# Kernel optimization log

Hardware: AMD Instinct MI355X
Metric: run time of the kernel (lower is better)

The kernel has to match this reference:

```python
import jax, jax.numpy as jnp
import numpy as np

TEMPERATURE = 0.1


def setup_inputs() -> dict:
    key = jax.random.key(0)
    k1, k2 = jax.random.split(key)
    B, D = 4096, 128
    z_i = jax.random.normal(k1, (B, D), dtype=jnp.float32)
    z_j = jax.random.normal(k2, (B, D), dtype=jnp.float32)
    return {"z_i": z_i, "z_j": z_j}


def reference(z_i, z_j):
    B = z_i.shape[0]
    n = 2 * B
    z = jnp.concatenate([z_i, z_j], axis=0)            # [2B, D]
    sim = jnp.matmul(z, z.T) / TEMPERATURE             # [2B, 2B]
    # positives: diag(sim, +B) and diag(sim, -B)
    pos = jnp.concatenate([jnp.diagonal(sim, B), jnp.diagonal(sim, -B)])[:, None]  # [2B, 1]
    # negatives: sim with diagonal removed, row-wise -> [2B, 2B-1]
    # strided trick equivalent to sim[~eye].reshape(n, n-1)
    neg = sim.ravel()[:-1].reshape(n - 1, n + 1)[:, 1:].reshape(n, n - 1)
    logits = jnp.concatenate([pos, neg], axis=1)       # [2B, 2B]
    # cross-entropy with labels all zero (positive in column 0)
    loss = jnp.mean(jax.nn.logsumexp(logits, axis=1) - logits[:, 0])
    return loss
```

## Files before the change

### kernel.cpp

```cpp
#include <hip/hip_runtime.h>
#include <hip/hip_bf16.h>
#include <stdint.h>

#define N_TOT  8192
#define BHALF  4096
#define DDIM   128
#define NSPLIT 16

typedef short bf16x8 __attribute__((ext_vector_type(8)));
typedef float f32x4  __attribute__((ext_vector_type(4)));

__device__ __forceinline__ float ex2(float x) { return __builtin_amdgcn_exp2f(x); }

#define SCALE_C 3.798282440185f

__device__ __forceinline__ ushort2 cvt2(float a, float b) {
    __hip_bfloat162 h = __float22bfloat162_rn(make_float2(a, b));
    return *reinterpret_cast<ushort2*>(&h);
}

__device__ __forceinline__ bf16x8 cvt8(float4 lo, float4 hi) {
    union { bf16x8 v; ushort2 u[4]; } r;
    r.u[0] = cvt2(lo.x * SCALE_C, lo.y * SCALE_C);
    r.u[1] = cvt2(lo.z * SCALE_C, lo.w * SCALE_C);
    r.u[2] = cvt2(hi.x * SCALE_C, hi.y * SCALE_C);
    r.u[3] = cvt2(hi.z * SCALE_C, hi.w * SCALE_C);
    return r.v;
}

struct StageRegs { float4 v[4]; };

__device__ __forceinline__ StageRegs stage_load(const float* __restrict__ zi,
                                                const float* __restrict__ zj,
                                                int colBase, int ch, int tid) {
    StageRegs s;
    #pragma unroll
    for (int it = 0; it < 2; ++it) {
        int idx  = it * 512 + tid;
        int col  = idx >> 4, g = idx & 15;
        int gcol = colBase + ch * 64 + col;
        const float* cp = (gcol < BHALF) ? zi + gcol * DDIM
                                         : zj + (gcol - BHALF) * DDIM;
        s.v[it * 2]     = *reinterpret_cast<const float4*>(cp + g * 8);
        s.v[it * 2 + 1] = *reinterpret_cast<const float4*>(cp + g * 8 + 4);
    }
    return s;
}

__device__ __forceinline__ void stage_write(const StageRegs& s, int tid,
                                            unsigned short* buf) {
    #pragma unroll
    for (int it = 0; it < 2; ++it) {
        int idx  = it * 512 + tid;
        int col  = idx >> 4, g = idx & 15;
        int slot = g ^ (col & 7);
        *reinterpret_cast<bf16x8*>(&buf[col * 128 + slot * 8]) =
            cvt8(s.v[it * 2], s.v[it * 2 + 1]);
    }
}

__launch_bounds__(512, 4)
__global__ void k_main(const float* __restrict__ zi, const float* __restrict__ zj,
                       float* __restrict__ pm, float* __restrict__ pl,
                       float* __restrict__ out) {
    if (blockIdx.x == 0 && threadIdx.x == 0) out[0] = 0.f;
    __shared__ unsigned short lds[2][64 * 128];
    const int tid = threadIdx.x;
    const int w = tid >> 6, lane = tid & 63;
    const int q = lane >> 4, ln = lane & 15;
    const int rb = blockIdx.x >> 4, cs = blockIdx.x & 15;
    const int rowBase = rb * 256 + w * 32;
    const int colBase = cs * 512;

    bf16x8 afr[2][4];
    #pragma unroll
    for (int s = 0; s < 2; ++s) {
        int row = rowBase + s * 16 + ln;
        const float* rp = (row < BHALF) ? zi + row * DDIM
                                        : zj + (row - BHALF) * DDIM;
        #pragma unroll
        for (int kc = 0; kc < 4; ++kc) {
            float4 lo = *reinterpret_cast<const float4*>(rp + kc * 32 + q * 8);
            float4 hi = *reinterpret_cast<const float4*>(rp + kc * 32 + q * 8 + 4);
            afr[s][kc] = cvt8(lo, hi);
        }
    }

    float m[2][4], l[2][4];
    #pragma unroll
    for (int s = 0; s < 2; ++s)
        #pragma unroll
        for (int r = 0; r < 4; ++r) { m[s][r] = -1e38f; l[s][r] = 0.f; }

    StageRegs sr = stage_load(zi, zj, colBase, 0, tid);
    stage_write(sr, tid, lds[0]);
    __syncthreads();

    for (int ch = 0; ch < 8; ++ch) {
        const unsigned short* buf = lds[ch & 1];
        if (ch < 7) sr = stage_load(zi, zj, colBase, ch + 1, tid);

        #pragma unroll
        for (int ct2 = 0; ct2 < 2; ++ct2) {
            f32x4 acc[2][2];
            #pragma unroll
            for (int s = 0; s < 2; ++s)
                #pragma unroll
                for (int u = 0; u < 2; ++u) acc[s][u] = (f32x4){0.f, 0.f, 0.f, 0.f};

            #pragma unroll
            for (int u = 0; u < 2; ++u) {
                int ct = ct2 * 2 + u;
                bf16x8 bfr[4];
                #pragma unroll
                for (int kc = 0; kc < 4; ++kc) {
                    int slot = (q + 4 * kc) ^ (ln & 7);
                    bfr[kc] = *reinterpret_cast<const bf16x8*>(
                        &buf[(ct * 16 + ln) * 128 + slot * 8]);
                }
                #pragma unroll
                for (int s = 0; s < 2; ++s)
                    #pragma unroll
                    for (int kc = 0; kc < 4; ++kc)
                        acc[s][u] = __builtin_amdgcn_mfma_f32_16x16x32_bf16(
                            afr[s][kc], bfr[kc], acc[s][u], 0, 0, 0);
            }

            const int c0 = colBase + ch * 64 + ct2 * 32;
            #pragma unroll
            for (int s = 0; s < 2; ++s) {
                const int rt = rowBase + s * 16;
                if (c0 == rt) {
                    #pragma unroll
                    for (int r = 0; r < 4; ++r)
                        if (ln == q * 4 + r) acc[s][0][r] = -__builtin_inff();
                } else if (c0 + 16 == rt) {
                    #pragma unroll
                    for (int r = 0; r < 4; ++r)
                        if (ln == q * 4 + r) acc[s][1][r] = -__builtin_inff();
                }
                #pragma unroll
                for (int r = 0; r < 4; ++r) {
                    float t0 = acc[s][0][r], t1 = acc[s][1][r];
                    float mo = m[s][r];
                    float mn = fmaxf(fmaxf(t0, t1), mo);
                    float sc = ex2(mo - mn);
                    float pv = ex2(t0 - mn) + ex2(t1 - mn);
                    l[s][r] = fmaf(l[s][r], sc, pv);
                    m[s][r] = mn;
                }
            }
        }

        if (ch < 7) stage_write(sr, tid, lds[(ch + 1) & 1]);
        __syncthreads();
    }

    #pragma unroll
    for (int s = 0; s < 2; ++s) {
        #pragma unroll
        for (int r = 0; r < 4; ++r) {
            float mm = m[s][r], ll = l[s][r];
            #pragma unroll
            for (int msk = 1; msk < 16; msk <<= 1) {
                float om = __shfl_xor(mm, msk, 64);
                float ol = __shfl_xor(ll, msk, 64);
                float mn = fmaxf(mm, om);
                ll = ll * ex2(mm - mn) + ol * ex2(om - mn);
                mm = mn;
            }
            if (ln == 0) {
                int row = rowBase + s * 16 + q * 4 + r;
                pm[cs * N_TOT + row] = mm;
                pl[cs * N_TOT + row] = ll;
            }
        }
    }
}

__global__ void k_finish(const float* __restrict__ zi, const float* __restrict__ zj,
                         const float* __restrict__ pm, const float* __restrict__ pl,
                         float* __restrict__ out) {
    int row = blockIdx.x * 256 + threadIdx.x;
    int pr  = row & (BHALF - 1);
    const float4* a = reinterpret_cast<const float4*>(zi + pr * DDIM);
    const float4* b = reinterpret_cast<const float4*>(zj + pr * DDIM);
    float acc = 0.f;
    #pragma unroll
    for (int k = 0; k < 32; ++k) {
        float4 x = a[k], y = b[k];
        acc += x.x * y.x + x.y * y.y + x.z * y.z + x.w * y.w;
    }
    float p  = 10.f * acc;
    float tp = p * 1.4426950408889634f;
    float mm[NSPLIT];
    float M = tp;
    #pragma unroll
    for (int j = 0; j < NSPLIT; ++j) {
        mm[j] = pm[j * N_TOT + row];
        M = fmaxf(M, mm[j]);
    }
    float S = ex2(tp - M);
    #pragma unroll
    for (int j = 0; j < NSPLIT; ++j)
        S += pl[j * N_TOT + row] * ex2(mm[j] - M);
    float lse = (M + __log2f(S)) * 0.6931471805599453f;
    float li  = lse - p;
    #pragma unroll
    for (int msk = 32; msk; msk >>= 1) li += __shfl_xor(li, msk, 64);
    __shared__ float red[4];
    if ((threadIdx.x & 63) == 0) red[threadIdx.x >> 6] = li;
    __syncthreads();
    if (threadIdx.x == 0)
        atomicAdd(out, (red[0] + red[1] + red[2] + red[3]) * (1.f / 8192.f));
}

extern "C" void kernel_launch(void* const* d_in, const int* in_sizes, int n_in,
                              void* d_out, int out_size, void* d_ws, size_t ws_size,
                              hipStream_t stream) {
    const float* zi = (const float*)d_in[0];
    const float* zj = (const float*)d_in[1];
    float* out = (float*)d_out;
    char* ws = (char*)d_ws;

    float* pm = (float*)ws;
    float* pl = pm + NSPLIT * N_TOT;

    hipLaunchKernelGGL(k_main,   dim3(512), dim3(512), 0, stream, zi, zj, pm, pl, out);
    hipLaunchKernelGGL(k_finish, dim3(32),  dim3(256), 0, stream, zi, zj, pm, pl, out);
}
```

Measured before the change: 99.78 us.

## Pre-convert inputs to swizzled bf16 and stage tiles via direct global-to-LDS loads

Adds a prep kernel that converts z_i/z_j once into a pre-swizzled bf16 buffer. The main kernel then fills its LDS tiles with global_load_lds DMA instead of loading fp32 into registers, converting, and writing to LDS. The loop is also restructured so each chunk processes four 16-column tiles before one online-softmax update instead of two pairs. This removes repeated per-block conversion and halves the bytes the main kernel reads, at the cost of an extra kernel launch and a workspace round-trip.

```diff
diff --git a/kernel.cpp b/kernel.cpp
--- a/kernel.cpp
+++ b/kernel.cpp
@@ -28,42 +28,28 @@
     return r.v;
 }
 
-struct StageRegs { float4 v[4]; };
-
-__device__ __forceinline__ StageRegs stage_load(const float* __restrict__ zi,
-                                                const float* __restrict__ zj,
-                                                int colBase, int ch, int tid) {
-    StageRegs s;
-    #pragma unroll
-    for (int it = 0; it < 2; ++it) {
-        int idx  = it * 512 + tid;
-        int col  = idx >> 4, g = idx & 15;
-        int gcol = colBase + ch * 64 + col;
-        const float* cp = (gcol < BHALF) ? zi + gcol * DDIM
-                                         : zj + (gcol - BHALF) * DDIM;
-        s.v[it * 2]     = *reinterpret_cast<const float4*>(cp + g * 8);
-        s.v[it * 2 + 1] = *reinterpret_cast<const float4*>(cp + g * 8 + 4);
-    }
-    return s;
-}
-
-__device__ __forceinline__ void stage_write(const StageRegs& s, int tid,
-                                            unsigned short* buf) {
-    #pragma unroll
-    for (int it = 0; it < 2; ++it) {
-        int idx  = it * 512 + tid;
-        int col  = idx >> 4, g = idx & 15;
-        int slot = g ^ (col & 7);
-        *reinterpret_cast<bf16x8*>(&buf[col * 128 + slot * 8]) =
-            cvt8(s.v[it * 2], s.v[it * 2 + 1]);
-    }
+__device__ __forceinline__ void gload16(const void* g, void* l) {
+    __builtin_amdgcn_global_load_lds(
+        (const __attribute__((address_space(1))) void*)g,
+        (__attribute__((address_space(3))) void*)l, 16, 0, 0);
+}
+
+__launch_bounds__(256)
+__global__ void k_prep(const float* __restrict__ zi, const float* __restrict__ zj,
+                       unsigned short* __restrict__ zb, float* __restrict__ out) {
+    if (blockIdx.x == 0 && threadIdx.x == 0) out[0] = 0.f;
+    int gid = blockIdx.x * 256 + threadIdx.x;
+    int row = gid >> 4, g = gid & 15;
+    const float* rp = (row < BHALF) ? zi + row * DDIM : zj + (row - BHALF) * DDIM;
+    float4 lo = *reinterpret_cast<const float4*>(rp + g * 8);
+    float4 hi = *reinterpret_cast<const float4*>(rp + g * 8 + 4);
+    int slot = g ^ (row & 7);
+    *reinterpret_cast<bf16x8*>(&zb[row * DDIM + slot * 8]) = cvt8(lo, hi);
 }
 
 __launch_bounds__(512, 4)
-__global__ void k_main(const float* __restrict__ zi, const float* __restrict__ zj,
-                       float* __restrict__ pm, float* __restrict__ pl,
-                       float* __restrict__ out) {
-    if (blockIdx.x == 0 && threadIdx.x == 0) out[0] = 0.f;
+__global__ void k_main(const unsigned short* __restrict__ zb,
+                       float* __restrict__ pm, float* __restrict__ pl) {
     __shared__ unsigned short lds[2][64 * 128];
     const int tid = threadIdx.x;
     const int w = tid >> 6, lane = tid & 63;
@@ -76,14 +62,11 @@
     #pragma unroll
     for (int s = 0; s < 2; ++s) {
         int row = rowBase + s * 16 + ln;
-        const float* rp = (row < BHALF) ? zi + row * DDIM
-                                        : zj + (row - BHALF) * DDIM;
-        #pragma unroll
-        for (int kc = 0; kc < 4; ++kc) {
-            float4 lo = *reinterpret_cast<const float4*>(rp + kc * 32 + q * 8);
-            float4 hi = *reinterpret_cast<const float4*>(rp + kc * 32 + q * 8 + 4);
-            afr[s][kc] = cvt8(lo, hi);
-        }
+        const unsigned short* rp = zb + row * DDIM;
+        int rx = row & 7;
+        #pragma unroll
+        for (int kc = 0; kc < 4; ++kc)
+            afr[s][kc] = *reinterpret_cast<const bf16x8*>(rp + ((kc * 4 + q) ^ rx) * 8);
     }
 
     float m[2][4], l[2][4];
@@ -92,69 +75,69 @@
         #pragma unroll
         for (int r = 0; r < 4; ++r) { m[s][r] = -1e38f; l[s][r] = 0.f; }
 
-    StageRegs sr = stage_load(zi, zj, colBase, 0, tid);
-    stage_write(sr, tid, lds[0]);
+#define STAGE(B, CH) do {                                                     \
+        const unsigned short* sp_ = zb + (colBase + (CH) * 64) * DDIM;        \
+        gload16(sp_ + (0 * 512 + tid) * 8, &lds[B][0 * 4096 + w * 512]);      \
+        gload16(sp_ + (1 * 512 + tid) * 8, &lds[B][1 * 4096 + w * 512]);      \
+    } while (0)
+
+    STAGE(0, 0);
     __syncthreads();
 
     for (int ch = 0; ch < 8; ++ch) {
         const unsigned short* buf = lds[ch & 1];
-        if (ch < 7) sr = stage_load(zi, zj, colBase, ch + 1, tid);
-
-        #pragma unroll
-        for (int ct2 = 0; ct2 < 2; ++ct2) {
-            f32x4 acc[2][2];
+        if (ch < 7) STAGE((ch + 1) & 1, ch + 1);
+
+        f32x4 acc[2][4];
+        #pragma unroll
+        for (int s = 0; s < 2; ++s)
+            #pragma unroll
+            for (int ct = 0; ct < 4; ++ct) acc[s][ct] = (f32x4){0.f, 0.f, 0.f, 0.f};
+
+        #pragma unroll
+        for (int ct = 0; ct < 4; ++ct) {
+            bf16x8 bfr[4];
+            #pragma unroll
+            for (int kc = 0; kc < 4; ++kc) {
+                int slot = (q + 4 * kc) ^ (ln & 7);
+                bfr[kc] = *reinterpret_cast<const bf16x8*>(
+                    &buf[(ct * 16 + ln) * 128 + slot * 8]);
+            }
             #pragma unroll
             for (int s = 0; s < 2; ++s)
                 #pragma unroll
-                for (int u = 0; u < 2; ++u) acc[s][u] = (f32x4){0.f, 0.f, 0.f, 0.f};
-
-            #pragma unroll
-            for (int u = 0; u < 2; ++u) {
-                int ct = ct2 * 2 + u;
-                bf16x8 bfr[4];
-                #pragma unroll
-                for (int kc = 0; kc < 4; ++kc) {
-                    int slot = (q + 4 * kc) ^ (ln & 7);
-                    bfr[kc] = *reinterpret_cast<const bf16x8*>(
-                        &buf[(ct * 16 + ln) * 128 + slot * 8]);
-                }
-                #pragma unroll
-                for (int s = 0; s < 2; ++s)
-                    #pragma unroll
-                    for (int kc = 0; kc < 4; ++kc)
-                        acc[s][u] = __builtin_amdgcn_mfma_f32_16x16x32_bf16(
-                            afr[s][kc], bfr[kc], acc[s][u], 0, 0, 0);
-            }
-
-            const int c0 = colBase + ch * 64 + ct2 * 32;
-            #pragma unroll
-            for (int s = 0; s < 2; ++s) {
-                const int rt = rowBase + s * 16;
-                if (c0 == rt) {
+                for (int kc = 0; kc < 4; ++kc)
+                    acc[s][ct] = __builtin_amdgcn_mfma_f32_16x16x32_bf16(
+                        afr[s][kc], bfr[kc], acc[s][ct], 0, 0, 0);
+        }
+
+        const int c0 = colBase + ch * 64;
+        #pragma unroll
+        for (int s = 0; s < 2; ++s) {
+            const int rt = rowBase + s * 16;
+            #pragma unroll
+            for (int ct = 0; ct < 4; ++ct) {
+                if (rt == c0 + ct * 16) {
                     #pragma unroll
                     for (int r = 0; r < 4; ++r)
-                        if (ln == q * 4 + r) acc[s][0][r] = -__builtin_inff();
-                } else if (c0 + 16 == rt) {
-                    #pragma unroll
-                    for (int r = 0; r < 4; ++r)
-                        if (ln == q * 4 + r) acc[s][1][r] = -__builtin_inff();
+                        if (ln == q * 4 + r) acc[s][ct][r] = -__builtin_inff();
                 }
-                #pragma unroll
-                for (int r = 0; r < 4; ++r) {
-                    float t0 = acc[s][0][r], t1 = acc[s][1][r];
-                    float mo = m[s][r];
-                    float mn = fmaxf(fmaxf(t0, t1), mo);
-                    float sc = ex2(mo - mn);
-                    float pv = ex2(t0 - mn) + ex2(t1 - mn);
-                    l[s][r] = fmaf(l[s][r], sc, pv);
-                    m[s][r] = mn;
-                }
+            }
+            #pragma unroll
+            for (int r = 0; r < 4; ++r) {
+                float t0 = acc[s][0][r], t1 = acc[s][1][r];
+                float t2 = acc[s][2][r], t3 = acc[s][3][r];
+                float mo = m[s][r];
+                float mn = fmaxf(fmaxf(fmaxf(t0, t1), fmaxf(t2, t3)), mo);
+                float sc = ex2(mo - mn);
+                float pv = (ex2(t0 - mn) + ex2(t1 - mn)) + (ex2(t2 - mn) + ex2(t3 - mn));
+                l[s][r] = fmaf(l[s][r], sc, pv);
+                m[s][r] = mn;
             }
         }
-
-        if (ch < 7) stage_write(sr, tid, lds[(ch + 1) & 1]);
         __syncthreads();
     }
+#undef STAGE
 
     #pragma unroll
     for (int s = 0; s < 2; ++s) {
@@ -223,9 +206,11 @@
     float* out = (float*)d_out;
     char* ws = (char*)d_ws;
 
-    float* pm = (float*)ws;
+    unsigned short* zb = (unsigned short*)ws;
+    float* pm = (float*)(ws + (size_t)N_TOT * DDIM * 2);
     float* pl = pm + NSPLIT * N_TOT;
 
-    hipLaunchKernelGGL(k_main,   dim3(512), dim3(512), 0, stream, zi, zj, pm, pl, out);
+    hipLaunchKernelGGL(k_prep,   dim3(512), dim3(256), 0, stream, zi, zj, zb, out);
+    hipLaunchKernelGGL(k_main,   dim3(512), dim3(512), 0, stream, zb, pm, pl);
     hipLaunchKernelGGL(k_finish, dim3(32),  dim3(256), 0, stream, zi, zj, pm, pl, out);
 }
```

Result: faster. 96.13 us (-3.7%).
